# Optimization experiments

Measured on AMD Instinct MI355X. Metric: run time of the kernel, lower is better.

## Reference

```python
import jax, jax.numpy as jnp
import numpy as np

NEG_SLOPE = 0.1
BN_EPS = 1e-5

def lrelu(z):
    return jax.nn.leaky_relu(z, NEG_SLOPE)

def conv1d(x, w, b):
    # x: [B,C,L], w: [O,I,K], 'same' padding for K=3
    y = jax.lax.conv_general_dilated(x, w, (1,), [(1, 1)], dimension_numbers=('NCH', 'OIH', 'NCH'))
    return y + b[None, :, None]

def batchnorm_train(x, g, be):
    # training-mode BatchNorm1d over (B, L) per channel; x: [B,C,L]
    m = x.mean(axis=(0, 2), keepdims=True)
    v = x.var(axis=(0, 2), keepdims=True)
    return g[None, :, None] * (x - m) * jax.lax.rsqrt(v + BN_EPS) + be[None, :, None]

def setup_inputs() -> dict:
    key = jax.random.key(0)
    ks = jax.random.split(key, 16)
    L, B, E = 100, 32, 512
    F, K, M, H, DEC = 256, 3, 128, 512, 512
    D = F + 2  # cnn feats + 2 coord dims
    s = 0.02
    inp = {
        'x': jax.random.normal(ks[0], (L, B, E), jnp.float32),
        'h': jax.random.normal(ks[1], (B, H), jnp.float32),
        'cw1': jax.random.normal(ks[2], (F, E, K), jnp.float32) * s,
        'cb1': jnp.zeros((F,), jnp.float32),
        'g1': jnp.ones((F,), jnp.float32), 'be1': jnp.zeros((F,), jnp.float32),
        'cw2': jax.random.normal(ks[3], (F, F, K), jnp.float32) * s,
        'cb2': jnp.zeros((F,), jnp.float32),
        'g2': jnp.ones((F,), jnp.float32), 'be2': jnp.zeros((F,), jnp.float32),
        'cw3': jax.random.normal(ks[4], (F, F, K), jnp.float32) * s,
        'cb3': jnp.zeros((F,), jnp.float32),
        'g3': jnp.ones((F,), jnp.float32), 'be3': jnp.zeros((F,), jnp.float32),
        'cw4': jax.random.normal(ks[5], (F, F, K), jnp.float32) * s,
        'cb4': jnp.zeros((F,), jnp.float32),
        'g4': jnp.ones((F,), jnp.float32), 'be4': jnp.zeros((F,), jnp.float32),
        'W1': jax.random.normal(ks[6], (2 * D + H, M), jnp.float32) * s,
        'b1': jnp.zeros((M,), jnp.float32),
        'W2': jax.random.normal(ks[7], (M, M), jnp.float32) * s,
        'b2': jnp.zeros((M,), jnp.float32),
        'W3': jax.random.normal(ks[8], (M, M), jnp.float32) * s,
        'b3': jnp.zeros((M,), jnp.float32),
        'W4': jax.random.normal(ks[9], (M, M), jnp.float32) * s,
        'b4': jnp.zeros((M,), jnp.float32),
        'F1': jax.random.normal(ks[10], (M, M), jnp.float32) * s,
        'fb1': jnp.zeros((M,), jnp.float32),
        'F2': jax.random.normal(ks[11], (M, DEC), jnp.float32) * s,
        'fb2': jnp.zeros((DEC,), jnp.float32),
    }
    return inp

def reference(x, h, cw1, cb1, g1, be1, cw2, cb2, g2, be2, cw3, cb3, g3, be3,
              cw4, cb4, g4, be4, W1, b1, W2, b2, W3, b3, W4, b4, F1, fb1, F2, fb2):
    # x: [L,B,E] -> [B,E,L]
    xc = jnp.transpose(x, (1, 2, 0))
    for cw, cb, g, be in ((cw1, cb1, g1, be1), (cw2, cb2, g2, be2),
                          (cw3, cb3, g3, be3), (cw4, cb4, g4, be4)):
        xc = batchnorm_train(lrelu(conv1d(xc, cw, cb)), g, be)
    xc = jnp.transpose(xc, (0, 2, 1))  # [B,L,F]
    B, L, _ = xc.shape
    # coordinate tensor: cvt_coord(i, L) = [(i/sqrt(L)-2)/2, (i%sqrt(L)-2)/2]
    i = jnp.arange(L, dtype=jnp.float32)
    sL = jnp.sqrt(jnp.float32(L))
    coord = jnp.stack([(i / sL - 2.0) / 2.0, (jnp.mod(i, sL) - 2.0) / 2.0], axis=-1)
    xf = jnp.concatenate([xc, jnp.broadcast_to(coord, (B, L, 2))], axis=-1)  # [B,L,D]
    D = xf.shape[-1]
    # pair[b,i,j] = [xf[b,j], xf[b,i], h[b]]; split W1 to avoid materializing concat
    Wa, Wb, Wc = W1[:D], W1[D:2 * D], W1[2 * D:]
    A = xf @ Wa                              # contribution of x_j, [B,L,M]
    C = xf @ Wb + (h @ Wc + b1)[:, None, :]  # contribution of x_i and h, [B,L,M]
    g = lrelu(C[:, :, None, :] + A[:, None, :, :])  # [B,L,L,M]
    g = lrelu(g @ W2 + b2)
    g = lrelu(g @ W3 + b3)
    g = lrelu(g @ W4 + b4)
    s = g.sum(axis=(1, 2))  # sum-pool over all L*L pairs -> [B,M]
    out = lrelu(lrelu(s @ F1 + fb1) @ F2 + fb2)  # [B,dec_hid]
    return out
```

## Files before the change

### kernel.cpp

```cpp
#include <hip/hip_runtime.h>
#include <hip/hip_bf16.h>
#include <stdint.h>
#include <stddef.h>

#define NEG 0.1f

typedef __attribute__((ext_vector_type(8))) short short8;
typedef __attribute__((ext_vector_type(16))) float floatx16;

__device__ __forceinline__ unsigned f2bf(float f) {
  union { float f; unsigned u; } v; v.f = f;
  unsigned r = v.u + 0x7FFFu + ((v.u >> 16) & 1u);
  return r >> 16;
}
__device__ __forceinline__ unsigned pk2bf(float a, float b) {
  __hip_bfloat162 hh = __float22bfloat162_rn(make_float2(a, b));
  union { __hip_bfloat162 h; unsigned u; } v; v.h = hh; return v.u;
}
__device__ __forceinline__ float bits2f(unsigned u) {
  union { unsigned u; float f; } v; v.u = u; return v.f;
}

__global__ void k_prep(const float* __restrict__ cw1, const float* __restrict__ cw2,
                       const float* __restrict__ cw3, const float* __restrict__ cw4,
                       unsigned short* __restrict__ wt1, unsigned short* __restrict__ wt2,
                       unsigned short* __restrict__ wt3, unsigned short* __restrict__ wt4,
                       const float* __restrict__ W1, unsigned short* __restrict__ wab,
                       const float* __restrict__ W2, const float* __restrict__ W3,
                       const float* __restrict__ W4, unsigned short* __restrict__ wmlp,
                       const float* __restrict__ h, float* __restrict__ hc) {
  __shared__ float tile[64 * 65];
  int bid = blockIdx.x, tid = threadIdx.x;
  if (bid < 1280) {
    int z = bid;
    int E; const float* cw; unsigned short* wt;
    if (z < 512) { E = 512; cw = cw1; wt = wt1; }
    else {
      int q = (z - 512) >> 8; E = 256;
      cw = (q == 0) ? cw2 : ((q == 1) ? cw3 : cw4);
      wt = (q == 0) ? wt2 : ((q == 1) ? wt3 : wt4);
      z = (z - 512) & 255;
    }
    int idx = z * 256 + tid;
    int f = idx / E, e = idx - f * E;
    const float* s = cw + (size_t)idx * 3;
    unsigned short* d = wt + (size_t)f * 3 * E + e;
    d[0] = (unsigned short)f2bf(s[0]);
    d[E] = (unsigned short)f2bf(s[1]);
    d[2 * E] = (unsigned short)f2bf(s[2]);
  } else if (bid < 1304) {
    int tw = bid - 1280;
    int half = tw / 12, rem = tw % 12, dt = rem >> 1, nt = rem & 1;
    int c = tid & 63, rq = tid >> 6;
#pragma unroll
    for (int it = 0; it < 16; ++it) {
      int r = rq + it * 4;
      int kp = dt * 64 + r;
      float v = 0.f;
      if (kp < 258) v = W1[(size_t)(half * 258 + kp) * 128 + nt * 64 + c];
      tile[r * 65 + c] = v;
    }
    __syncthreads();
#pragma unroll
    for (int it = 0; it < 16; ++it) {
      int r2 = rq + it * 4;
      wab[(size_t)(half * 128 + nt * 64 + r2) * 384 + dt * 64 + c] =
          (unsigned short)f2bf(tile[c * 65 + r2]);
    }
  } else if (bid < 1496) {
    int i2 = (bid - 1304) * 256 + tid;
    int n = i2 & 127, k = (i2 >> 7) & 127, zz = i2 >> 14;
    const float* W = (zz == 0) ? W2 : ((zz == 1) ? W3 : W4);
    float v = W[k * 128 + n];
    int w = n >> 5, l = ((k >> 3) & 1) * 32 + (n & 31), kk = k >> 4, j = k & 7;
    int i = (((zz * 4 + w) * 8 + kk) << 9) | (l << 3) | j;
    wmlp[i] = (unsigned short)f2bf(v);
  } else {
    int t = bid - 1496;
    int b = t >> 2, seg = t & 3;
    int m = tid & 127, sub = tid >> 7;
    int k0 = seg * 128 + sub * 64;
    const float* hr = h + b * 512 + k0;
    const float* Wc = W1 + (size_t)(516 + k0) * 128 + m;
    float a0 = 0.f, a1 = 0.f, a2 = 0.f, a3 = 0.f, a4 = 0.f, a5 = 0.f, a6 = 0.f, a7 = 0.f;
#pragma unroll
    for (int k = 0; k < 64; k += 8) {
      a0 += hr[k + 0] * Wc[(size_t)(k + 0) * 128];
      a1 += hr[k + 1] * Wc[(size_t)(k + 1) * 128];
      a2 += hr[k + 2] * Wc[(size_t)(k + 2) * 128];
      a3 += hr[k + 3] * Wc[(size_t)(k + 3) * 128];
      a4 += hr[k + 4] * Wc[(size_t)(k + 4) * 128];
      a5 += hr[k + 5] * Wc[(size_t)(k + 5) * 128];
      a6 += hr[k + 6] * Wc[(size_t)(k + 6) * 128];
      a7 += hr[k + 7] * Wc[(size_t)(k + 7) * 128];
    }
    float s = ((a0 + a1) + (a2 + a3)) + ((a4 + a5) + (a6 + a7));
    atomicAdd(&hc[b * 128 + m], s);
  }
}

__global__ __launch_bounds__(256, 2) void k_conv(
    const float* __restrict__ zin, const float* __restrict__ bnin,
    const float* __restrict__ gamv, const float* __restrict__ betv,
    const unsigned short* __restrict__ wt, const float* __restrict__ cb,
    float* __restrict__ zout, float* __restrict__ bnout, int E, int xmode) {
  extern __shared__ unsigned short smem[];
  const int SL = (E == 512) ? 520 : 264;
  unsigned short* slab = smem;
  unsigned short* Bs = smem + 34 * SL;
  const int K = 3 * E, NC = K >> 6, NCH = NC >> 1;
  const int esh = (E == 512) ? 9 : 8;
  int tid = threadIdx.x;
  int lane = tid & 63, wave = tid >> 6;
  int khalf = wave >> 1, cwave = wave & 1;
  int r0 = blockIdx.x * 32, ct = blockIdx.y;
  int i32 = lane & 31;
  int koff = (lane >> 5) << 3;

  int lrow = (r0 + i32) % 100;
  bool vks0 = (lrow >= 1), vks2 = (lrow <= 98);

  if (xmode) {
    for (int s = wave; s < 34; s += 4) {
      int m = r0 - 1 + s; m = min(max(m, 0), 3199);
      int b = m / 100, l = m - b * 100;
      size_t base = (size_t)(l * 32 + b) * 512;
#pragma unroll
      for (int cc = 0; cc < 2; ++cc) {
        int ch = cc * 256 + lane * 4;
        float4 v = *(const float4*)(zin + base + ch);
        uint2 p; p.x = pk2bf(v.x, v.y); p.y = pk2bf(v.z, v.w);
        *(uint2*)(&slab[s * SL + ch]) = p;
      }
    }
  } else {
    const float inv = 1.f / 3200.f;
    float sc[4], sh[4];
#pragma unroll
    for (int q = 0; q < 4; ++q) {
      int ch = lane * 4 + q;
      float mme = bnin[ch] * inv;
      float var = bnin[256 + ch] * inv - mme * mme;
      sc[q] = gamv[ch] * rsqrtf(var + 1e-5f);
      sh[q] = betv[ch] - mme * sc[q];
    }
    for (int s = wave; s < 34; s += 4) {
      int m = r0 - 1 + s; m = min(max(m, 0), 3199);
      float4 v = *(const float4*)(zin + (size_t)m * 256 + lane * 4);
      uint2 p;
      p.x = pk2bf(v.x * sc[0] + sh[0], v.y * sc[1] + sh[1]);
      p.y = pk2bf(v.z * sc[2] + sh[2], v.w * sc[3] + sh[3]);
      *(uint2*)(&slab[s * SL + lane * 4]) = p;
    }
  }

  floatx16 acc;
#pragma unroll
  for (int q = 0; q < 16; ++q) acc[q] = 0.f;

  int t128 = tid & 127;
  int brow = t128 >> 1, bhalf = (t128 & 1) * 32;
  const unsigned short* wrow = wt + (size_t)(ct * 64 + brow) * K + khalf * NCH * 64 + bhalf;
  uint4 pre[4];
#pragma unroll
  for (int t = 0; t < 4; ++t) pre[t] = *(const uint4*)(wrow + t * 8);

  for (int c = 0; c < NCH; ++c) {
    unsigned short* Bc = Bs + (khalf * 2 + (c & 1)) * (64 * 72);
#pragma unroll
    for (int t = 0; t < 4; ++t)
      *(uint4*)(&Bc[brow * 72 + bhalf + t * 8]) = pre[t];
    __syncthreads();
    if (c + 1 < NCH) {
#pragma unroll
      for (int t = 0; t < 4; ++t)
        pre[t] = *(const uint4*)(wrow + (c + 1) * 64 + t * 8);
    }
    int cg = khalf * NCH + c;
    int ks = (cg << 6) >> esh;
    int ebase = (cg << 6) & (E - 1);
    bool v = (ks == 0) ? vks0 : ((ks == 2) ? vks2 : true);
    int srow = i32 + ks;
#pragma unroll
    for (int kk = 0; kk < 4; ++kk) {
      short8 a = {};
      if (v) a = *(const short8*)(&slab[srow * SL + ebase + kk * 16 + koff]);
      short8 b8 = *(const short8*)(&Bc[(cwave * 32 + i32) * 72 + kk * 16 + koff]);
      acc = __builtin_amdgcn_mfma_f32_32x32x16_bf16(a, b8, acc, 0, 0, 0);
    }
  }

  __syncthreads();
  float* scr = (float*)smem;
  if (khalf == 1) {
#pragma unroll
    for (int reg = 0; reg < 16; ++reg) {
      int rowp = (reg & 3) + 8 * (reg >> 2) + 4 * (lane >> 5);
      scr[cwave * 1024 + rowp * 32 + i32] = acc[reg];
    }
  }
  __syncthreads();
  if (khalf == 0) {
    int f = ct * 64 + cwave * 32 + i32;
    float bias = cb[f];
    float s1 = 0.f, s2 = 0.f;
#pragma unroll
    for (int reg = 0; reg < 16; ++reg) {
      int rowp = (reg & 3) + 8 * (reg >> 2) + 4 * (lane >> 5);
      int m = r0 + rowp;
      float v = acc[reg] + scr[cwave * 1024 + rowp * 32 + i32] + bias;
      v = fmaxf(v, NEG * v);
      zout[(size_t)m * 256 + f] = v;
      s1 += v; s2 += v * v;
    }
    s1 += __shfl_xor(s1, 32, 64);
    s2 += __shfl_xor(s2, 32, 64);
    if (lane < 32) { atomicAdd(&bnout[f], s1); atomicAdd(&bnout[256 + f], s2); }
  }
}

__global__ __launch_bounds__(128, 2) void k_ac(
    const float* __restrict__ zin, const float* __restrict__ bnin,
    const float* __restrict__ gamv, const float* __restrict__ betv,
    const unsigned short* __restrict__ wab, const float* __restrict__ hc,
    const float* __restrict__ b1v,
    unsigned short* __restrict__ Abf, unsigned short* __restrict__ Cbf) {
  __shared__ unsigned short slab[32 * 328];
  __shared__ unsigned short Bs[2 * 64 * 72];
  int tid = threadIdx.x;
  int lane = tid & 63, wave = tid >> 6;
  int r0 = blockIdx.x * 32, ct = blockIdx.y;
  int i32 = lane & 31;
  int koff = (lane >> 5) << 3;
  const float inv = 1.f / 3200.f;

  {
    float sc[4], sh[4];
#pragma unroll
    for (int q = 0; q < 4; ++q) {
      int ch = lane * 4 + q;
      float mme = bnin[ch] * inv;
      float var = bnin[256 + ch] * inv - mme * mme;
      sc[q] = gamv[ch] * rsqrtf(var + 1e-5f);
      sh[q] = betv[ch] - mme * sc[q];
    }
    for (int s = wave; s < 32; s += 2) {
      int m = r0 + s;
      float4 v = *(const float4*)(zin + (size_t)m * 256 + lane * 4);
      uint2 p;
      p.x = pk2bf(v.x * sc[0] + sh[0], v.y * sc[1] + sh[1]);
      p.y = pk2bf(v.z * sc[2] + sh[2], v.w * sc[3] + sh[3]);
      *(uint2*)(&slab[s * 328 + lane * 4]) = p;
    }
    if (wave == 0) {
      int s = i32, half = (lane >> 5) * 32;
      int m = r0 + s, l = m % 100;
      float c0 = ((float)l * 0.1f - 2.0f) * 0.5f;
      float c1 = ((float)(l % 10) - 2.0f) * 0.5f;
#pragma unroll
      for (int seg = 0; seg < 4; ++seg) {
        uint4 z4; z4.x = z4.y = z4.z = z4.w = 0u;
        if (half == 0 && seg == 0) z4.x = pk2bf(c0, c1);
        *(uint4*)(&slab[s * 328 + 256 + half + seg * 8]) = z4;
      }
    }
  }

  floatx16 acc;
#pragma unroll
  for (int q = 0; q < 16; ++q) acc[q] = 0.f;

  int brow = tid >> 1, bhalf = (tid & 1) * 32;
  uint4 pre[4];
#pragma unroll
  for (int t = 0; t < 4; ++t)
    pre[t] = *(const uint4*)(wab + (size_t)(ct * 64 + brow) * 384 + bhalf + t * 8);

  for (int c = 0; c < 5; ++c) {
    unsigned short* Bc = Bs + (c & 1) * (64 * 72);
#pragma unroll
    for (int t = 0; t < 4; ++t)
      *(uint4*)(&Bc[brow * 72 + bhalf + t * 8]) = pre[t];
    __syncthreads();
    if (c + 1 < 5) {
#pragma unroll
      for (int t = 0; t < 4; ++t)
        pre[t] = *(const uint4*)(wab + (size_t)(ct * 64 + brow) * 384 + (c + 1) * 64 + bhalf + t * 8);
    }
#pragma unroll
    for (int kk = 0; kk < 4; ++kk) {
      short8 a = *(const short8*)(&slab[i32 * 328 + c * 64 + kk * 16 + koff]);
      short8 b8 = *(const short8*)(&Bc[(wave * 32 + i32) * 72 + kk * 16 + koff]);
      acc = __builtin_amdgcn_mfma_f32_32x32x16_bf16(a, b8, acc, 0, 0, 0);
    }
  }

  int n = ct * 64 + wave * 32 + i32;
#pragma unroll
  for (int reg = 0; reg < 16; ++reg) {
    int rowp = (reg & 3) + 8 * (reg >> 2) + 4 * (lane >> 5);
    int m = r0 + rowp;
    float v = acc[reg];
    if (ct < 2) {
      Abf[(size_t)m * 128 + n] = (unsigned short)f2bf(v);
    } else {
      int b = m / 100;
      int nc = n - 128;
      Cbf[(size_t)m * 128 + nc] =
          (unsigned short)f2bf(v + hc[b * 128 + nc] + b1v[nc]);
    }
  }
}

__global__ __launch_bounds__(256, 2) void k_mlp(
    const unsigned short* __restrict__ Abf, const unsigned short* __restrict__ Cbf,
    const unsigned short* __restrict__ wmlp, const float* __restrict__ b2,
    const float* __restrict__ b3, const float* __restrict__ b4,
    float* __restrict__ sout) {
  __shared__ unsigned short gs0[128 * 128];
  __shared__ unsigned short gs1[128 * 128];
  int tid = threadIdx.x, lane = tid & 63, wave = tid >> 6;
  int ln31 = lane & 31;
  int half = lane >> 5;
  int rx = ln31 & 15;

  short8 wreg[3][8];
#pragma unroll
  for (int z = 0; z < 3; ++z)
#pragma unroll
    for (int kk = 0; kk < 8; ++kk)
      wreg[z][kk] = *(const short8*)(wmlp + (size_t)(((z * 4 + wave) * 8 + kk) * 512) + lane * 8);

  int wb = wave * 32;
  float4 bq[2][4];
#pragma unroll
  for (int q = 0; q < 4; ++q) {
    bq[0][q] = *(const float4*)(b2 + wb + q * 8 + 4 * half);
    bq[1][q] = *(const float4*)(b3 + wb + q * 8 + 4 * half);
  }
  float bv4 = b4[wb + ln31];

  for (int ti = 0; ti < 2; ++ti) {
    int t = blockIdx.x + ti * 1264;
    int b = t / 79, tt = t - b * 79;
    __syncthreads();
    {
      int lr = wb + (lane >> 1);
      int hh = lane & 1;
      int lbase = lr * 128, lrx = lr & 15;
      int r = tt * 128 + lr;
      if (r > 9999) r = 9999;
      const unsigned short* Crow = Cbf + (size_t)(b * 100 + r / 100) * 128;
      const unsigned short* Arow = Abf + (size_t)(b * 100 + r % 100) * 128;
#pragma unroll
      for (int it = 0; it < 8; ++it) {
        int cc = hh * 64 + it * 8;
        uint4 c4 = *(const uint4*)(Crow + cc);
        uint4 a4 = *(const uint4*)(Arow + cc);
        unsigned cw[4] = {c4.x, c4.y, c4.z, c4.w};
        unsigned aw[4] = {a4.x, a4.y, a4.z, a4.w};
        unsigned ow[4];
#pragma unroll
        for (int q = 0; q < 4; ++q) {
          float x0 = bits2f(cw[q] << 16) + bits2f(aw[q] << 16);
          float x1 = bits2f(cw[q] & 0xFFFF0000u) + bits2f(aw[q] & 0xFFFF0000u);
          x0 = fmaxf(x0, NEG * x0);
          x1 = fmaxf(x1, NEG * x1);
          ow[q] = pk2bf(x0, x1);
        }
        uint4 o4; o4.x = ow[0]; o4.y = ow[1]; o4.z = ow[2]; o4.w = ow[3];
        *(uint4*)(&gs0[lbase + (((hh * 8 + it) ^ lrx) << 3)]) = o4;
      }
    }
    __syncthreads();

#pragma unroll
    for (int z = 0; z < 2; ++z) {
      const unsigned short* src = z ? gs1 : gs0;
      unsigned short* dst = z ? gs0 : gs1;
#pragma unroll
      for (int rg = 0; rg < 4; ++rg) {
        floatx16 acc;
#pragma unroll
        for (int q = 0; q < 16; ++q) acc[q] = 0.f;
        int rowb = (rg * 32 + ln31) * 128;
#pragma unroll
        for (int kk = 0; kk < 8; ++kk) {
          short8 g8 = *(const short8*)(&src[rowb + (((kk * 2 + half) ^ rx) << 3)]);
          acc = __builtin_amdgcn_mfma_f32_32x32x16_bf16(wreg[z][kk], g8, acc, 0, 0, 0);
        }
        int pr = rg * 32 + ln31;
        int prb = pr * 128;
#pragma unroll
        for (int q = 0; q < 4; ++q) {
          float4 bb = bq[z][q];
          float v0 = acc[q * 4 + 0] + bb.x; v0 = fmaxf(v0, NEG * v0);
          float v1 = acc[q * 4 + 1] + bb.y; v1 = fmaxf(v1, NEG * v1);
          float v2 = acc[q * 4 + 2] + bb.z; v2 = fmaxf(v2, NEG * v2);
          float v3 = acc[q * 4 + 3] + bb.w; v3 = fmaxf(v3, NEG * v3);
          uint2 p; p.x = pk2bf(v0, v1); p.y = pk2bf(v2, v3);
          *(uint2*)(&dst[prb + (((wave * 4 + q) ^ rx) << 3) + half * 4]) = p;
        }
      }
      __syncthreads();
    }

    float colsum = 0.f;
#pragma unroll
    for (int rg = 0; rg < 4; ++rg) {
      floatx16 acc;
#pragma unroll
      for (int q = 0; q < 16; ++q) acc[q] = 0.f;
      int rowb = (rg * 32 + ln31) * 128;
#pragma unroll
      for (int kk = 0; kk < 8; ++kk) {
        short8 a8 = *(const short8*)(&gs0[rowb + (((kk * 2 + half) ^ rx) << 3)]);
        acc = __builtin_amdgcn_mfma_f32_32x32x16_bf16(a8, wreg[2][kk], acc, 0, 0, 0);
      }
#pragma unroll
      for (int reg = 0; reg < 16; ++reg) {
        int rowp = (reg & 3) + 8 * (reg >> 2) + 4 * half;
        int p = tt * 128 + rg * 32 + rowp;
        float v = acc[reg] + bv4;
        v = fmaxf(v, NEG * v);
        colsum += (p < 10000) ? v : 0.f;
      }
    }
    colsum += __shfl_xor(colsum, 32, 64);
    if (lane < 32) atomicAdd(&sout[b * 128 + wb + lane], colsum);
  }
}

__global__ void k_final(const float* __restrict__ s, const float* __restrict__ F1,
                        const float* __restrict__ fb1, const float* __restrict__ F2,
                        const float* __restrict__ fb2, float* __restrict__ out) {
  __shared__ float sl[128], t1[128];
  int b = blockIdx.x, t = threadIdx.x;
  if (t < 128) sl[t] = s[b * 128 + t];
  __syncthreads();
  if (t < 128) {
    float a = fb1[t];
    for (int k = 0; k < 128; ++k) a += sl[k] * F1[k * 128 + t];
    t1[t] = fmaxf(a, NEG * a);
  }
  __syncthreads();
  for (int o = t; o < 512; o += 256) {
    float a = fb2[o];
    for (int k = 0; k < 128; ++k) a += t1[k] * F2[k * 512 + o];
    out[b * 512 + o] = fmaxf(a, NEG * a);
  }
}

extern "C" void kernel_launch(void* const* d_in, const int* in_sizes, int n_in,
                              void* d_out, int out_size, void* d_ws, size_t ws_size,
                              hipStream_t stream) {
  const float* x   = (const float*)d_in[0];
  const float* h   = (const float*)d_in[1];
  const float* cw1 = (const float*)d_in[2];
  const float* cb1 = (const float*)d_in[3];
  const float* g1  = (const float*)d_in[4];
  const float* be1 = (const float*)d_in[5];
  const float* cw2 = (const float*)d_in[6];
  const float* cb2 = (const float*)d_in[7];
  const float* g2  = (const float*)d_in[8];
  const float* be2 = (const float*)d_in[9];
  const float* cw3 = (const float*)d_in[10];
  const float* cb3 = (const float*)d_in[11];
  const float* g3  = (const float*)d_in[12];
  const float* be3 = (const float*)d_in[13];
  const float* cw4 = (const float*)d_in[14];
  const float* cb4 = (const float*)d_in[15];
  const float* g4  = (const float*)d_in[16];
  const float* be4 = (const float*)d_in[17];
  const float* W1  = (const float*)d_in[18];
  const float* b1  = (const float*)d_in[19];
  const float* W2  = (const float*)d_in[20];
  const float* b2  = (const float*)d_in[21];
  const float* W3  = (const float*)d_in[22];
  const float* b3  = (const float*)d_in[23];
  const float* W4  = (const float*)d_in[24];
  const float* b4  = (const float*)d_in[25];
  const float* F1  = (const float*)d_in[26];
  const float* fb1 = (const float*)d_in[27];
  const float* F2  = (const float*)d_in[28];
  const float* fb2 = (const float*)d_in[29];

  char* ws = (char*)d_ws;
  float* bn0  = (float*)(ws + 0);
  float* bn1  = (float*)(ws + 2048);
  float* bn2  = (float*)(ws + 4096);
  float* bn3  = (float*)(ws + 6144);
  float* sbuf = (float*)(ws + 8192);
  float* hc   = (float*)(ws + 24576);
  float* za   = (float*)(ws + 40960);
  float* zb   = (float*)(ws + 3317760);
  unsigned short* wt1  = (unsigned short*)(ws + 6594560);
  unsigned short* wt2  = (unsigned short*)(ws + 7380992);
  unsigned short* wt3  = (unsigned short*)(ws + 7774208);
  unsigned short* wt4  = (unsigned short*)(ws + 8167424);
  unsigned short* wab  = (unsigned short*)(ws + 8560640);
  unsigned short* wmlp = (unsigned short*)(ws + 8757248);
  unsigned short* Abf  = (unsigned short*)(ws + 8855552);
  unsigned short* Cbf  = (unsigned short*)(ws + 9674752);

  hipMemsetAsync(d_ws, 0, 40960, stream);

  k_prep<<<1624, 256, 0, stream>>>(cw1, cw2, cw3, cw4, wt1, wt2, wt3, wt4,
                                   W1, wab, W2, W3, W4, wmlp, h, hc);

  const int lds1 = (34 * 520 + 4 * 64 * 72) * 2;
  const int lds2 = (34 * 264 + 4 * 64 * 72) * 2;
  k_conv<<<dim3(100, 4), 256, lds1, stream>>>(x,  nullptr, nullptr, nullptr, wt1, cb1, za, bn0, 512, 1);
  k_conv<<<dim3(100, 4), 256, lds2, stream>>>(za, bn0, g1, be1, wt2, cb2, zb, bn1, 256, 0);
  k_conv<<<dim3(100, 4), 256, lds2, stream>>>(zb, bn1, g2, be2, wt3, cb3, za, bn2, 256, 0);
  k_conv<<<dim3(100, 4), 256, lds2, stream>>>(za, bn2, g3, be3, wt4, cb4, zb, bn3, 256, 0);

  k_ac<<<dim3(100, 4), 128, 0, stream>>>(zb, bn3, g4, be4, wab, hc, b1, Abf, Cbf);

  k_mlp<<<1264, 256, 0, stream>>>(Abf, Cbf, wmlp, b2, b3, b4, sbuf);
  k_final<<<32, 256, 0, stream>>>(sbuf, F1, fb1, F2, fb2, (float*)d_out);
}
```

Baseline: 284.4 us.

## Keep MLP activations in registers per wave, stage weights in LDS

Restructures the pairwise MLP kernel so each wave owns 32 pair rows and chains all three layers in registers. Layer outputs are rearranged with permlane32_swap instead of round-tripping through LDS with block-wide barriers. The three weight matrices and biases move from per-wave registers into LDS, loaded once per 1024-thread block, and the grid becomes 256 persistent blocks looping over work units. This removes the LDS activation traffic and syncs, but every MFMA now needs a weight fragment read from LDS, and the atomic count grows because each wave issues its own partial sums.

```diff
diff --git a/kernel.cpp b/kernel.cpp
--- a/kernel.cpp
+++ b/kernel.cpp
@@ -312,122 +312,126 @@
   }
 }
 
-__global__ __launch_bounds__(256, 2) void k_mlp(
+__device__ __forceinline__ void mlp_layer(const int z, const unsigned short* wlds,
+                                          const float* bias_lds, const int lane,
+                                          const int h, const short8 (&gin)[8],
+                                          short8 (&gout)[8]) {
+#pragma unroll
+  for (int a = 0; a < 4; ++a) {
+    floatx16 acc;
+#pragma unroll
+    for (int q = 0; q < 16; ++q) acc[q] = 0.f;
+#pragma unroll
+    for (int kk = 0; kk < 8; ++kk) {
+      short8 wf = *(const short8*)(wlds + (((z * 4 + a) * 8 + kk) << 9) + lane * 8);
+      acc = __builtin_amdgcn_mfma_f32_32x32x16_bf16(wf, gin[kk], acc, 0, 0, 0);
+    }
+#pragma unroll
+    for (int qg = 0; qg < 4; ++qg) {
+      float4 bb = *(const float4*)(bias_lds + z * 128 + a * 32 + qg * 8 + h * 4);
+      float v0 = acc[qg * 4 + 0] + bb.x;
+      float v1 = acc[qg * 4 + 1] + bb.y;
+      float v2 = acc[qg * 4 + 2] + bb.z;
+      float v3 = acc[qg * 4 + 3] + bb.w;
+      acc[qg * 4 + 0] = fmaxf(v0, NEG * v0);
+      acc[qg * 4 + 1] = fmaxf(v1, NEG * v1);
+      acc[qg * 4 + 2] = fmaxf(v2, NEG * v2);
+      acc[qg * 4 + 3] = fmaxf(v3, NEG * v3);
+    }
+#pragma unroll
+    for (int c = 0; c < 2; ++c) {
+      unsigned X0 = pk2bf(acc[8 * c + 0], acc[8 * c + 1]);
+      unsigned X1 = pk2bf(acc[8 * c + 2], acc[8 * c + 3]);
+      unsigned Y0 = pk2bf(acc[8 * c + 4], acc[8 * c + 5]);
+      unsigned Y1 = pk2bf(acc[8 * c + 6], acc[8 * c + 7]);
+      auto p0 = __builtin_amdgcn_permlane32_swap(X0, Y0, false, false);
+      auto p1 = __builtin_amdgcn_permlane32_swap(X1, Y1, false, false);
+      union { unsigned w[4]; short8 s; } uu;
+      uu.w[0] = (unsigned)p0[0]; uu.w[1] = (unsigned)p1[0];
+      uu.w[2] = (unsigned)p0[1]; uu.w[3] = (unsigned)p1[1];
+      gout[2 * a + c] = uu.s;
+    }
+  }
+}
+
+__global__ __launch_bounds__(1024, 4) void k_mlp(
     const unsigned short* __restrict__ Abf, const unsigned short* __restrict__ Cbf,
     const unsigned short* __restrict__ wmlp, const float* __restrict__ b2,
     const float* __restrict__ b3, const float* __restrict__ b4,
     float* __restrict__ sout) {
-  __shared__ unsigned short gs0[128 * 128];
-  __shared__ unsigned short gs1[128 * 128];
+  extern __shared__ unsigned short wsm[];
+  float* bias_lds = (float*)(wsm + 49152);
   int tid = threadIdx.x, lane = tid & 63, wave = tid >> 6;
-  int ln31 = lane & 31;
-  int half = lane >> 5;
-  int rx = ln31 & 15;
-
-  short8 wreg[3][8];
-#pragma unroll
-  for (int z = 0; z < 3; ++z)
-#pragma unroll
-    for (int kk = 0; kk < 8; ++kk)
-      wreg[z][kk] = *(const short8*)(wmlp + (size_t)(((z * 4 + wave) * 8 + kk) * 512) + lane * 8);
-
-  int wb = wave * 32;
-  float4 bq[2][4];
-#pragma unroll
-  for (int q = 0; q < 4; ++q) {
-    bq[0][q] = *(const float4*)(b2 + wb + q * 8 + 4 * half);
-    bq[1][q] = *(const float4*)(b3 + wb + q * 8 + 4 * half);
-  }
-  float bv4 = b4[wb + ln31];
-
-  for (int ti = 0; ti < 2; ++ti) {
-    int t = blockIdx.x + ti * 1264;
-    int b = t / 79, tt = t - b * 79;
-    __syncthreads();
-    {
-      int lr = wb + (lane >> 1);
-      int hh = lane & 1;
-      int lbase = lr * 128, lrx = lr & 15;
-      int r = tt * 128 + lr;
-      if (r > 9999) r = 9999;
-      const unsigned short* Crow = Cbf + (size_t)(b * 100 + r / 100) * 128;
-      const unsigned short* Arow = Abf + (size_t)(b * 100 + r % 100) * 128;
-#pragma unroll
-      for (int it = 0; it < 8; ++it) {
-        int cc = hh * 64 + it * 8;
-        uint4 c4 = *(const uint4*)(Crow + cc);
-        uint4 a4 = *(const uint4*)(Arow + cc);
-        unsigned cw[4] = {c4.x, c4.y, c4.z, c4.w};
-        unsigned aw[4] = {a4.x, a4.y, a4.z, a4.w};
-        unsigned ow[4];
-#pragma unroll
-        for (int q = 0; q < 4; ++q) {
-          float x0 = bits2f(cw[q] << 16) + bits2f(aw[q] << 16);
-          float x1 = bits2f(cw[q] & 0xFFFF0000u) + bits2f(aw[q] & 0xFFFF0000u);
-          x0 = fmaxf(x0, NEG * x0);
-          x1 = fmaxf(x1, NEG * x1);
-          ow[q] = pk2bf(x0, x1);
-        }
-        uint4 o4; o4.x = ow[0]; o4.y = ow[1]; o4.z = ow[2]; o4.w = ow[3];
-        *(uint4*)(&gs0[lbase + (((hh * 8 + it) ^ lrx) << 3)]) = o4;
+  int ln31 = lane & 31, h = lane >> 5;
+
+  {
+    const uint4* s4 = (const uint4*)wmlp;
+    uint4* d4 = (uint4*)wsm;
+#pragma unroll
+    for (int i = 0; i < 6; ++i) d4[tid + i * 1024] = s4[tid + i * 1024];
+    if (tid < 256) bias_lds[tid] = (tid < 128) ? b2[tid] : b3[tid - 128];
+  }
+  float b4v[4];
+#pragma unroll
+  for (int a = 0; a < 4; ++a) b4v[a] = b4[a * 32 + ln31];
+  __syncthreads();
+
+  int slot = blockIdx.x * 16 + wave;
+  for (int it = 0; it < 3; ++it) {
+    int u = it * 4096 + slot;
+    if (u >= 10016) break;
+    int b = u / 313, lu = u - b * 313;
+    int r = lu * 32 + ln31;
+    int rc = min(r, 9999);
+    int i = rc / 100, j = rc - i * 100;
+    const unsigned short* Crow = Cbf + (size_t)(b * 100 + i) * 128 + h * 8;
+    const unsigned short* Arow = Abf + (size_t)(b * 100 + j) * 128 + h * 8;
+
+    short8 ga[8], gb[8];
+#pragma unroll
+    for (int kk = 0; kk < 8; ++kk) {
+      uint4 c4 = *(const uint4*)(Crow + kk * 16);
+      uint4 a4 = *(const uint4*)(Arow + kk * 16);
+      unsigned cw[4] = {c4.x, c4.y, c4.z, c4.w};
+      unsigned aw[4] = {a4.x, a4.y, a4.z, a4.w};
+      unsigned ow[4];
+#pragma unroll
+      for (int q = 0; q < 4; ++q) {
+        float x0 = bits2f(cw[q] << 16) + bits2f(aw[q] << 16);
+        float x1 = bits2f(cw[q] & 0xFFFF0000u) + bits2f(aw[q] & 0xFFFF0000u);
+        x0 = fmaxf(x0, NEG * x0);
+        x1 = fmaxf(x1, NEG * x1);
+        ow[q] = pk2bf(x0, x1);
       }
-    }
-    __syncthreads();
-
-#pragma unroll
-    for (int z = 0; z < 2; ++z) {
-      const unsigned short* src = z ? gs1 : gs0;
-      unsigned short* dst = z ? gs0 : gs1;
-#pragma unroll
-      for (int rg = 0; rg < 4; ++rg) {
-        floatx16 acc;
-#pragma unroll
-        for (int q = 0; q < 16; ++q) acc[q] = 0.f;
-        int rowb = (rg * 32 + ln31) * 128;
-#pragma unroll
-        for (int kk = 0; kk < 8; ++kk) {
-          short8 g8 = *(const short8*)(&src[rowb + (((kk * 2 + half) ^ rx) << 3)]);
-          acc = __builtin_amdgcn_mfma_f32_32x32x16_bf16(wreg[z][kk], g8, acc, 0, 0, 0);
-        }
-        int pr = rg * 32 + ln31;
-        int prb = pr * 128;
-#pragma unroll
-        for (int q = 0; q < 4; ++q) {
-          float4 bb = bq[z][q];
-          float v0 = acc[q * 4 + 0] + bb.x; v0 = fmaxf(v0, NEG * v0);
-          float v1 = acc[q * 4 + 1] + bb.y; v1 = fmaxf(v1, NEG * v1);
-          float v2 = acc[q * 4 + 2] + bb.z; v2 = fmaxf(v2, NEG * v2);
-          float v3 = acc[q * 4 + 3] + bb.w; v3 = fmaxf(v3, NEG * v3);
-          uint2 p; p.x = pk2bf(v0, v1); p.y = pk2bf(v2, v3);
-          *(uint2*)(&dst[prb + (((wave * 4 + q) ^ rx) << 3) + half * 4]) = p;
-        }
+      union { unsigned w[4]; short8 s; } uu;
+      uu.w[0] = ow[0]; uu.w[1] = ow[1]; uu.w[2] = ow[2]; uu.w[3] = ow[3];
+      ga[kk] = uu.s;
+    }
+
+    mlp_layer(0, wsm, bias_lds, lane, h, ga, gb);
+    mlp_layer(1, wsm, bias_lds, lane, h, gb, ga);
+
+#pragma unroll
+    for (int a = 0; a < 4; ++a) {
+      floatx16 acc;
+#pragma unroll
+      for (int q = 0; q < 16; ++q) acc[q] = 0.f;
+#pragma unroll
+      for (int kk = 0; kk < 8; ++kk) {
+        short8 wf = *(const short8*)(wsm + (((8 + a) * 8 + kk) << 9) + lane * 8);
+        acc = __builtin_amdgcn_mfma_f32_32x32x16_bf16(ga[kk], wf, acc, 0, 0, 0);
       }
-      __syncthreads();
-    }
-
-    float colsum = 0.f;
-#pragma unroll
-    for (int rg = 0; rg < 4; ++rg) {
-      floatx16 acc;
-#pragma unroll
-      for (int q = 0; q < 16; ++q) acc[q] = 0.f;
-      int rowb = (rg * 32 + ln31) * 128;
-#pragma unroll
-      for (int kk = 0; kk < 8; ++kk) {
-        short8 a8 = *(const short8*)(&gs0[rowb + (((kk * 2 + half) ^ rx) << 3)]);
-        acc = __builtin_amdgcn_mfma_f32_32x32x16_bf16(a8, wreg[2][kk], acc, 0, 0, 0);
+      float s = 0.f;
+#pragma unroll
+      for (int reg = 0; reg < 16; ++reg) {
+        int rowp = (reg & 3) + 8 * (reg >> 2) + 4 * h;
+        float v = acc[reg] + b4v[a];
+        v = fmaxf(v, NEG * v);
+        s += (lu * 32 + rowp < 10000) ? v : 0.f;
       }
-#pragma unroll
-      for (int reg = 0; reg < 16; ++reg) {
-        int rowp = (reg & 3) + 8 * (reg >> 2) + 4 * half;
-        int p = tt * 128 + rg * 32 + rowp;
-        float v = acc[reg] + bv4;
-        v = fmaxf(v, NEG * v);
-        colsum += (p < 10000) ? v : 0.f;
-      }
-    }
-    colsum += __shfl_xor(colsum, 32, 64);
-    if (lane < 32) atomicAdd(&sout[b * 128 + wb + lane], colsum);
+      s += __shfl_xor(s, 32, 64);
+      if (lane < 32) atomicAdd(&sout[b * 128 + a * 32 + ln31], s);
+    }
   }
 }
 
@@ -517,6 +521,7 @@
 
   k_ac<<<dim3(100, 4), 128, 0, stream>>>(zb, bn3, g4, be4, wab, hc, b1, Abf, Cbf);
 
-  k_mlp<<<1264, 256, 0, stream>>>(Abf, Cbf, wmlp, b2, b3, b4, sbuf);
+  const int ldsm = 49152 * 2 + 256 * 4;
+  k_mlp<<<256, 1024, ldsm, stream>>>(Abf, Cbf, wmlp, b2, b3, b4, sbuf);
   k_final<<<32, 256, 0, stream>>>(sbuf, F1, fb1, F2, fb2, (float*)d_out);
 }
```

After: 280.8 us. About the same (-1.3%).
